# Optimization experiments

Hardware: AMD Instinct MI355X
Metric: run time of the kernel (lower is better)

Reference implementation:

```python
import jax, jax.numpy as jnp
import numpy as np

N_HEADS = 16
N_KV_HEADS = 4
HEAD_DIM = 128
ROPE_THETA = 10000.0


def _rope_cos_sin(seq_len, head_dim, dtype):
    inv_freq = 1.0 / (ROPE_THETA ** (jnp.arange(0, head_dim, 2, dtype=jnp.float32) / head_dim))
    angles = jnp.arange(seq_len, dtype=jnp.float32)[:, None] * inv_freq[None, :]  # [S, hd/2]
    return jnp.cos(angles).astype(dtype), jnp.sin(angles).astype(dtype)


def _apply_rope(t, cos, sin):
    # t: [B, S, H, hd]; interleaved-pair (complex) rotation, Llama style
    B, S, H, hd = t.shape
    tr = t.reshape(B, S, H, hd // 2, 2)
    t0, t1 = tr[..., 0], tr[..., 1]
    c = cos[None, :, None, :]
    s = sin[None, :, None, :]
    out = jnp.stack([t0 * c - t1 * s, t0 * s + t1 * c], axis=-1)
    return out.reshape(B, S, H, hd)


def setup_inputs() -> dict:
    key = jax.random.key(0)
    ks = jax.random.split(key, 5)
    B, S, D = 2, 2048, 2048
    scale = 0.02
    return {
        "x": jax.random.normal(ks[0], (B, S, D), dtype=jnp.float32),
        "wq": jax.random.normal(ks[1], (N_HEADS * HEAD_DIM, D), dtype=jnp.float32) * scale,
        "wk": jax.random.normal(ks[2], (N_KV_HEADS * HEAD_DIM, D), dtype=jnp.float32) * scale,
        "wv": jax.random.normal(ks[3], (N_KV_HEADS * HEAD_DIM, D), dtype=jnp.float32) * scale,
        "wo": jax.random.normal(ks[4], (D, N_HEADS * HEAD_DIM), dtype=jnp.float32) * scale,
    }


def reference(x, wq, wk, wv, wo):
    B, S, D = x.shape
    hd = HEAD_DIM
    # QKV projections (torch Linear: y = x @ W.T)
    q = (x @ wq.T).reshape(B, S, N_HEADS, hd)
    k = (x @ wk.T).reshape(B, S, N_KV_HEADS, hd)
    v = (x @ wv.T).reshape(B, S, N_KV_HEADS, hd)
    # RoPE on q, k
    cos, sin = _rope_cos_sin(S, hd, x.dtype)
    q = _apply_rope(q, cos, sin)
    k = _apply_rope(k, cos, sin)
    # GQA: repeat kv heads to match query heads
    rep = N_HEADS // N_KV_HEADS
    k = jnp.repeat(k, rep, axis=2)  # [B, S, H, hd]
    v = jnp.repeat(v, rep, axis=2)
    # Causal SDPA
    scores = jnp.einsum("bqhd,bkhd->bhqk", q, k) / jnp.sqrt(jnp.asarray(hd, x.dtype))
    causal = jnp.tril(jnp.ones((S, S), dtype=bool))
    scores = jnp.where(causal[None, None], scores, jnp.asarray(-1e30, x.dtype))
    attn = jax.nn.softmax(scores, axis=-1)
    out = jnp.einsum("bhqk,bkhd->bqhd", attn, v).reshape(B, S, N_HEADS * hd)
    return out @ wo.T
```

## Files before the change

kernel.cpp:

```cpp
#include <hip/hip_runtime.h>
#include <stdint.h>

typedef unsigned short u16;
typedef __attribute__((ext_vector_type(8))) __bf16 bf16x8;
typedef __attribute__((ext_vector_type(4))) float f32x4;

__device__ __forceinline__ u16 f2bf(float f) {
  union { float f; uint32_t u; } v; v.f = f;
  uint32_t u = v.u;
  uint32_t r = (u + 0x7fffu + ((u >> 16) & 1u)) >> 16;
  return (u16)r;
}
__device__ __forceinline__ float bf2f(u16 h) {
  union { uint32_t u; float f; } v; v.u = ((uint32_t)h) << 16;
  return v.f;
}

__device__ __forceinline__ void gld16(const void* g, void* l) {
  __builtin_amdgcn_global_load_lds(
      (__attribute__((address_space(1))) void*)(uintptr_t)g,
      (__attribute__((address_space(3))) void*)l,
      16, 0, 0);
}

__global__ __launch_bounds__(256) void cast_all(const float* __restrict__ x,
                                                const float* __restrict__ wq,
                                                const float* __restrict__ wk,
                                                const float* __restrict__ wv,
                                                const float* __restrict__ wo,
                                                u16* __restrict__ xb,
                                                u16* __restrict__ wqkv,
                                                u16* __restrict__ wob) {
  int i = blockIdx.x * 256 + threadIdx.x;
  const float* src; u16* dst; int loc, base;
  if (i < 2097152)      { src = x;  dst = xb;   loc = i;           base = 0; }
  else if (i < 3145728) { src = wq; dst = wqkv; loc = i - 2097152; base = 0; }
  else if (i < 3407872) { src = wk; dst = wqkv; loc = i - 3145728; base = 1048576; }
  else if (i < 3670016) { src = wv; dst = wqkv; loc = i - 3407872; base = 1310720; }
  else                  { src = wo; dst = wob;  loc = i - 3670016; base = 0; }
  float4 f = ((const float4*)src)[loc];
  ushort4 o;
  o.x = f2bf(f.x); o.y = f2bf(f.y); o.z = f2bf(f.z); o.w = f2bf(f.w);
  ((ushort4*)dst)[base + loc] = o;
}

__global__ __launch_bounds__(256) void gemm_bt(const u16* __restrict__ A,
                                               const u16* __restrict__ B,
                                               void* __restrict__ C,
                                               int M, int N, int K, int out_f32)
{
  __shared__ u16 As[128 * 64];
  __shared__ u16 Bs[128 * 64];
  const int tid  = threadIdx.x;
  const int wave = tid >> 6, lane = tid & 63;
  const int col  = lane & 15, quad = lane >> 4;
  const int bm = blockIdx.y, bn = blockIdx.x;
  const int wm = (wave >> 1) * 64, wn = (wave & 1) * 64;
  const size_t arow0 = (size_t)bm * 128, brow0 = (size_t)bn * 128;

  const int sr = lane >> 3, pc = lane & 7;

  const f32x4 fz = {0.f, 0.f, 0.f, 0.f};
  f32x4 acc[4][4];
  for (int i = 0; i < 4; ++i)
    for (int j = 0; j < 4; ++j) acc[i][j] = fz;

  for (int k0 = 0; k0 < K; k0 += 64) {
    __syncthreads();
    #pragma unroll
    for (int i = 0; i < 4; ++i) {
      int rA = wave * 32 + i * 8 + sr;
      int lc = pc ^ (rA & 7);
      gld16(A + (arow0 + rA) * K + k0 + lc * 8, As + (wave * 32 + i * 8) * 64);
      gld16(B + (brow0 + rA) * K + k0 + lc * 8, Bs + (wave * 32 + i * 8) * 64);
    }
    __syncthreads();
    #pragma unroll
    for (int kk = 0; kk < 2; ++kk) {
      const int swz = (((kk * 4 + quad) ^ (col & 7)) * 8);
      bf16x8 af[4];
      #pragma unroll
      for (int mt = 0; mt < 4; ++mt)
        af[mt] = *(const bf16x8*)&As[(wm + mt * 16 + col) * 64 + swz];
      #pragma unroll
      for (int nt = 0; nt < 4; ++nt) {
        bf16x8 bf = *(const bf16x8*)&Bs[(wn + nt * 16 + col) * 64 + swz];
        #pragma unroll
        for (int mt = 0; mt < 4; ++mt)
          acc[mt][nt] = __builtin_amdgcn_mfma_f32_16x16x32_bf16(af[mt], bf, acc[mt][nt], 0, 0, 0);
      }
    }
  }

  #pragma unroll
  for (int mt = 0; mt < 4; ++mt)
    #pragma unroll
    for (int nt = 0; nt < 4; ++nt)
      #pragma unroll
      for (int i = 0; i < 4; ++i) {
        size_t grow = arow0 + wm + mt * 16 + quad * 4 + i;
        size_t gcol = brow0 + wn + nt * 16 + col;
        float v = acc[mt][nt][i];
        if (out_f32) ((float*)C)[grow * N + gcol] = v;
        else         ((u16*)C)[grow * N + gcol]   = f2bf(v);
      }
}

__global__ __launch_bounds__(256) void rope_kernel(u16* __restrict__ t, int S, float qscale) {
  int idx = blockIdx.x * 256 + threadIdx.x;
  int i = idx & 63;
  int r = idx >> 6;
  int hh = r % 20; r /= 20;
  int s = r % S;
  int b = r / S;
  float inv = exp2f(-(float)i * 0.20762050593046f);
  float ang = (float)s * inv;
  float sn, cs;
  __sincosf(ang, &sn, &cs);
  int colb = (hh < 16) ? hh * 128 : 2048 + (hh - 16) * 128;
  float osc = (hh < 16) ? qscale : 1.0f;
  size_t base = (size_t)(b * S + s) * 3072 + colb + 2 * i;
  float t0 = bf2f(t[base]), t1 = bf2f(t[base + 1]);
  t[base]     = f2bf((t0 * cs - t1 * sn) * osc);
  t[base + 1] = f2bf((t0 * sn + t1 * cs) * osc);
}

__global__ __launch_bounds__(256) void vtrans_kernel(const u16* __restrict__ qkv,
                                                     u16* __restrict__ Vtg, int S) {
  __shared__ u16 T[64 * 65];
  const int s0 = blockIdx.x * 64, d0 = blockIdx.y * 64, bk = blockIdx.z;
  const int b = bk >> 2, kvh = bk & 3;
  const u16* src = qkv + (size_t)b * S * 3072 + 2560 + kvh * 128 + d0;
  #pragma unroll 4
  for (int it = 0; it < 16; ++it) {
    int idx = it * 256 + threadIdx.x;
    int r = idx >> 6, c = idx & 63;
    T[c * 65 + r] = src[(size_t)(s0 + r) * 3072 + c];
  }
  __syncthreads();
  #pragma unroll 4
  for (int it = 0; it < 16; ++it) {
    int idx = it * 256 + threadIdx.x;
    int d = idx >> 6, s = idx & 63;
    Vtg[((size_t)bk * 128 + d0 + d) * S + s0 + s] = T[d * 65 + s];
  }
}

__global__ __launch_bounds__(256, 2) void attn_kernel(const u16* __restrict__ QKV,
                                                      const u16* __restrict__ Vtg,
                                                      u16* __restrict__ Ctx,
                                                      int B, int S)
{
  const int x = blockIdx.x;
  const int t = x >> 5, bh = x & 31;
  const int qt = (x < 256) ? (15 - t) : (t - 8);
  const int h = bh & 15, b = bh >> 4;
  const int tid  = threadIdx.x;
  const int wave = tid >> 6, lane = tid & 63;
  const int col  = lane & 15, quad = lane >> 4;
  const int q0   = qt * 128;
  const int kvh  = h >> 2;
  const int row0w = q0 + wave * 32;

  __shared__ u16 Ks[2][64 * 128];
  __shared__ u16 Ps[4][32 * 72];

  bf16x8 aq[2][4];
  #pragma unroll
  for (int mt = 0; mt < 2; ++mt)
    #pragma unroll
    for (int ks = 0; ks < 4; ++ks)
      aq[mt][ks] = *(const bf16x8*)(QKV + (size_t)(b * S + row0w + mt * 16 + col) * 3072
                                        + h * 128 + ks * 32 + quad * 8);
  #pragma unroll
  for (int mt = 0; mt < 2; ++mt)
    #pragma unroll
    for (int ks = 0; ks < 4; ++ks)
      asm volatile("" :: "v"(__builtin_bit_cast(f32x4, aq[mt][ks])));

  const u16* KVb = QKV + (size_t)b * S * 3072 + 2048 + kvh * 128;
  const u16* Vtb = Vtg + ((size_t)(b * 4 + kvh) * 128) * S;
  u16* Pw = Ps[wave];

  const f32x4 fz = {0.f, 0.f, 0.f, 0.f};
  f32x4 o[2][8];
  #pragma unroll
  for (int mt = 0; mt < 2; ++mt)
    #pragma unroll
    for (int nc = 0; nc < 8; ++nc) o[mt][nc] = fz;
  float rs[2] = {0.f, 0.f};

  const int kt_max = 2 * qt + 1;

  #pragma unroll
  for (int i = 0; i < 4; ++i) {
    int r = wave * 16 + i * 4 + (lane >> 4);
    int lc = (lane & 15) ^ (r & 15);
    gld16(KVb + (size_t)r * 3072 + lc * 8, Ks[0] + (wave * 16 + i * 4) * 128);
  }
  __syncthreads();

  for (int kt = 0; kt <= kt_max; ++kt) {
    if (kt < kt_max) {
      u16* kdst = Ks[(kt + 1) & 1];
      #pragma unroll
      for (int i = 0; i < 4; ++i) {
        int r = wave * 16 + i * 4 + (lane >> 4);
        int lc = (lane & 15) ^ (r & 15);
        gld16(KVb + (size_t)((kt + 1) * 64 + r) * 3072 + lc * 8,
              kdst + (wave * 16 + i * 4) * 128);
      }
    }

    const bool active = (kt * 64 <= row0w + 31);
    if (active) {
      const bool need_mask = (kt * 64 + 63 > row0w);
      const u16* Kc = Ks[kt & 1];

      bf16x8 bv[8][2];
      #pragma unroll
      for (int nc = 0; nc < 8; ++nc)
        #pragma unroll
        for (int ks = 0; ks < 2; ++ks)
          bv[nc][ks] = *(const bf16x8*)(Vtb + (size_t)(nc * 16 + col) * S
                                            + kt * 64 + (ks * 4 + quad) * 8);

      #pragma unroll
      for (int nt = 0; nt < 4; ++nt) {
        bf16x8 kA[4];
        #pragma unroll
        for (int ks = 0; ks < 4; ++ks)
          kA[ks] = *(const bf16x8*)&Kc[(nt * 16 + col) * 128 + (((ks * 4 + quad) ^ col) * 8)];
        #pragma unroll
        for (int mt = 0; mt < 2; ++mt) {
          f32x4 st = fz;
          __builtin_amdgcn_s_setprio(1);
          #pragma unroll
          for (int ks = 0; ks < 4; ++ks)
            st = __builtin_amdgcn_mfma_f32_16x16x32_bf16(kA[ks], aq[mt][ks], st, 0, 0, 0);
          __builtin_amdgcn_s_setprio(0);
          float pv[4];
          const int kbase = kt * 64 + nt * 16 + quad * 4;
          const int qrow  = row0w + mt * 16 + col;
          #pragma unroll
          for (int i = 0; i < 4; ++i) {
            float s = st[i];
            if (need_mask && (kbase + i > qrow)) s = -__builtin_inff();
            pv[i] = exp2f(s);
          }
          rs[mt] += (pv[0] + pv[1]) + (pv[2] + pv[3]);
          uint32_t d0 = (__float_as_uint(pv[0]) >> 16) | (__float_as_uint(pv[1]) & 0xffff0000u);
          uint32_t d1 = (__float_as_uint(pv[2]) >> 16) | (__float_as_uint(pv[3]) & 0xffff0000u);
          uint2 dd; dd.x = d0; dd.y = d1;
          *(uint2*)&Pw[(mt * 16 + col) * 72 + nt * 16 + quad * 4] = dd;
        }
      }
      __asm__ volatile("" ::: "memory");

      bf16x8 ap[2][2];
      #pragma unroll
      for (int mt = 0; mt < 2; ++mt)
        #pragma unroll
        for (int ks = 0; ks < 2; ++ks)
          ap[mt][ks] = *(const bf16x8*)&Pw[(mt * 16 + col) * 72 + ks * 32 + quad * 8];
      #pragma unroll
      for (int nc = 0; nc < 8; ++nc) {
        #pragma unroll
        for (int ks = 0; ks < 2; ++ks) {
          __builtin_amdgcn_s_setprio(1);
          #pragma unroll
          for (int mt = 0; mt < 2; ++mt)
            o[mt][nc] = __builtin_amdgcn_mfma_f32_16x16x32_bf16(ap[mt][ks], bv[nc][ks], o[mt][nc], 0, 0, 0);
          __builtin_amdgcn_s_setprio(0);
        }
      }
    }

    __syncthreads();
  }

  #pragma unroll
  for (int mt = 0; mt < 2; ++mt) {
    float v = rs[mt];
    v += __shfl_xor(v, 16);
    v += __shfl_xor(v, 32);
    float lv[4];
    #pragma unroll
    for (int i = 0; i < 4; ++i)
      lv[i] = 1.0f / __shfl(v, quad * 4 + i);
    #pragma unroll
    for (int nc = 0; nc < 8; ++nc)
      #pragma unroll
      for (int i = 0; i < 4; ++i) {
        int qg = row0w + mt * 16 + quad * 4 + i;
        Ctx[(size_t)(b * S + qg) * 2048 + h * 128 + nc * 16 + col] =
            f2bf(o[mt][nc][i] * lv[i]);
      }
  }
}

extern "C" void kernel_launch(void* const* d_in, const int* in_sizes, int n_in,
                              void* d_out, int out_size, void* d_ws, size_t ws_size,
                              hipStream_t stream) {
  const int B = 2, S = 2048, D = 2048;
  const int M = B * S;
  const int NQKV = 3072;

  const float* x  = (const float*)d_in[0];
  const float* wq = (const float*)d_in[1];
  const float* wk = (const float*)d_in[2];
  const float* wv = (const float*)d_in[3];
  const float* wo = (const float*)d_in[4];

  char* ws = (char*)d_ws;
  u16* xb    = (u16*)ws; ws += (size_t)M * D * 2;
  u16* wqkvb = (u16*)ws; ws += (size_t)NQKV * D * 2;
  u16* wob   = (u16*)ws; ws += (size_t)D * D * 2;
  u16* qkvb  = (u16*)ws; ws += (size_t)M * NQKV * 2;
  u16* vtg   = (u16*)ws; ws += (size_t)B * 4 * 128 * S * 2;
  u16* ctx   = (u16*)ws; ws += (size_t)M * D * 2;

  cast_all<<<18432, 256, 0, stream>>>(x, wq, wk, wv, wo, xb, wqkvb, wob);

  gemm_bt<<<dim3(NQKV / 128, M / 128), 256, 0, stream>>>(xb, wqkvb, qkvb, M, NQKV, D, 0);

  const float qscale = 0.12751744515623627f;
  rope_kernel<<<(M * 20 * 64) / 256, 256, 0, stream>>>(qkvb, S, qscale);

  vtrans_kernel<<<dim3(S / 64, 2, B * 4), 256, 0, stream>>>(qkvb, vtg, S);

  attn_kernel<<<512, 256, 0, stream>>>(qkvb, vtg, ctx, B, S);

  gemm_bt<<<dim3(D / 128, M / 128), 256, 0, stream>>>(ctx, wob, d_out, M, D, D, 1);
}
```

Baseline: 347.4 us.

## Stage V tiles in LDS via async loads and split PV into halves

V^T tiles are now double-buffered into shared memory with global_load_lds alongside K, using a swizzled layout, instead of each wave reading V straight from global memory into registers. The QK/softmax/PV work is split into two halves of 32 keys, so the P scratch buffer shrinks and is XOR-swizzled, and fewer V registers are live at once. The barrier moves to the start of each iteration. This aims to cut redundant global V traffic and register pressure, at the cost of more LDS use (which may lower occupancy) and extra LDS reads.

```diff
diff --git a/kernel.cpp b/kernel.cpp
--- a/kernel.cpp
+++ b/kernel.cpp
@@ -3,6 +3,7 @@
 
 typedef unsigned short u16;
 typedef __attribute__((ext_vector_type(8))) __bf16 bf16x8;
+typedef __attribute__((ext_vector_type(4))) __bf16 bf16x4;
 typedef __attribute__((ext_vector_type(4))) float f32x4;
 
 __device__ __forceinline__ u16 f2bf(float f) {
@@ -163,7 +164,8 @@
   const int row0w = q0 + wave * 32;
 
   __shared__ u16 Ks[2][64 * 128];
-  __shared__ u16 Ps[4][32 * 72];
+  __shared__ u16 Vt[2][128 * 64];
+  __shared__ u16 Ps[4][32 * 32];
 
   bf16x8 aq[2][4];
   #pragma unroll
@@ -192,41 +194,56 @@
 
   const int kt_max = 2 * qt + 1;
 
+  const int krow = (lane >> 4);
+  const int kcol = (lane & 15);
+  const int vrow = (lane >> 3);
+  const int vcol = (lane & 7);
+
   #pragma unroll
   for (int i = 0; i < 4; ++i) {
-    int r = wave * 16 + i * 4 + (lane >> 4);
-    int lc = (lane & 15) ^ (r & 15);
+    int r = wave * 16 + i * 4 + krow;
+    int lc = kcol ^ (r & 15);
     gld16(KVb + (size_t)r * 3072 + lc * 8, Ks[0] + (wave * 16 + i * 4) * 128);
   }
-  __syncthreads();
+  #pragma unroll
+  for (int i = 0; i < 4; ++i) {
+    int r = wave * 32 + i * 8 + vrow;
+    int lc = vcol ^ (r & 7);
+    gld16(Vtb + (size_t)r * S + lc * 8, Vt[0] + (wave * 32 + i * 8) * 64);
+  }
 
   for (int kt = 0; kt <= kt_max; ++kt) {
+    __syncthreads();
+
     if (kt < kt_max) {
       u16* kdst = Ks[(kt + 1) & 1];
+      u16* vdst = Vt[(kt + 1) & 1];
       #pragma unroll
       for (int i = 0; i < 4; ++i) {
-        int r = wave * 16 + i * 4 + (lane >> 4);
-        int lc = (lane & 15) ^ (r & 15);
+        int r = wave * 16 + i * 4 + krow;
+        int lc = kcol ^ (r & 15);
         gld16(KVb + (size_t)((kt + 1) * 64 + r) * 3072 + lc * 8,
               kdst + (wave * 16 + i * 4) * 128);
       }
+      #pragma unroll
+      for (int i = 0; i < 4; ++i) {
+        int r = wave * 32 + i * 8 + vrow;
+        int lc = vcol ^ (r & 7);
+        gld16(Vtb + (size_t)r * S + (kt + 1) * 64 + lc * 8,
+              vdst + (wave * 32 + i * 8) * 64);
+      }
     }
 
-    const bool active = (kt * 64 <= row0w + 31);
-    if (active) {
-      const bool need_mask = (kt * 64 + 63 > row0w);
-      const u16* Kc = Ks[kt & 1];
-
-      bf16x8 bv[8][2];
-      #pragma unroll
-      for (int nc = 0; nc < 8; ++nc)
-        #pragma unroll
-        for (int ks = 0; ks < 2; ++ks)
-          bv[nc][ks] = *(const bf16x8*)(Vtb + (size_t)(nc * 16 + col) * S
-                                            + kt * 64 + (ks * 4 + quad) * 8);
-
-      #pragma unroll
-      for (int nt = 0; nt < 4; ++nt) {
+    if (kt * 64 > row0w + 31) continue;
+    const bool need_mask = (kt * 64 + 63 > row0w);
+    const u16* Kc = Ks[kt & 1];
+    const u16* Vc = Vt[kt & 1];
+
+    #pragma unroll
+    for (int half = 0; half < 2; ++half) {
+      #pragma unroll
+      for (int ntl = 0; ntl < 2; ++ntl) {
+        const int nt = half * 2 + ntl;
         bf16x8 kA[4];
         #pragma unroll
         for (int ks = 0; ks < 4; ++ks)
@@ -252,31 +269,30 @@
           uint32_t d0 = (__float_as_uint(pv[0]) >> 16) | (__float_as_uint(pv[1]) & 0xffff0000u);
           uint32_t d1 = (__float_as_uint(pv[2]) >> 16) | (__float_as_uint(pv[3]) & 0xffff0000u);
           uint2 dd; dd.x = d0; dd.y = d1;
-          *(uint2*)&Pw[(mt * 16 + col) * 72 + nt * 16 + quad * 4] = dd;
+          const int prow = mt * 16 + col;
+          *(uint2*)&Pw[prow * 32 + (((ntl * 4 + quad) ^ (col & 7)) * 4)] = dd;
         }
       }
       __asm__ volatile("" ::: "memory");
 
-      bf16x8 ap[2][2];
-      #pragma unroll
-      for (int mt = 0; mt < 2; ++mt)
+      bf16x8 ap[2];
+      #pragma unroll
+      for (int mt = 0; mt < 2; ++mt) {
+        const int prow = mt * 16 + col;
+        bf16x4 lo = *(const bf16x4*)&Pw[prow * 32 + (((quad * 2 + 0) ^ (col & 7)) * 4)];
+        bf16x4 hi = *(const bf16x4*)&Pw[prow * 32 + (((quad * 2 + 1) ^ (col & 7)) * 4)];
+        ap[mt] = __builtin_shufflevector(lo, hi, 0, 1, 2, 3, 4, 5, 6, 7);
+      }
+      #pragma unroll
+      for (int nc = 0; nc < 8; ++nc) {
+        bf16x8 bv = *(const bf16x8*)&Vc[(nc * 16 + col) * 64 + (((half * 4 + quad) ^ (col & 7)) * 8)];
+        __builtin_amdgcn_s_setprio(1);
         #pragma unroll
-        for (int ks = 0; ks < 2; ++ks)
-          ap[mt][ks] = *(const bf16x8*)&Pw[(mt * 16 + col) * 72 + ks * 32 + quad * 8];
-      #pragma unroll
-      for (int nc = 0; nc < 8; ++nc) {
-        #pragma unroll
-        for (int ks = 0; ks < 2; ++ks) {
-          __builtin_amdgcn_s_setprio(1);
-          #pragma unroll
-          for (int mt = 0; mt < 2; ++mt)
-            o[mt][nc] = __builtin_amdgcn_mfma_f32_16x16x32_bf16(ap[mt][ks], bv[nc][ks], o[mt][nc], 0, 0, 0);
-          __builtin_amdgcn_s_setprio(0);
-        }
+        for (int mt = 0; mt < 2; ++mt)
+          o[mt][nc] = __builtin_amdgcn_mfma_f32_16x16x32_bf16(ap[mt], bv, o[mt][nc], 0, 0, 0);
+        __builtin_amdgcn_s_setprio(0);
       }
     }
-
-    __syncthreads();
   }
 
   #pragma unroll
```

New measurement: 317.0 us. 1.1x faster.
